# Kernel optimization log

Measured on AMD Instinct MI355X. Metric: run time of the kernel, lower is better.

The kernel has to match this reference:

```python
import jax, jax.numpy as jnp
import numpy as np

NUM_SPECIAL = 3  # rows 1..NUM_SPECIAL in special table; row 0 is padding (zeros)

def setup_inputs() -> dict:
    key = jax.random.key(0)
    ks = jax.random.split(key, 16)
    T, B, E, H, L, V = 128, 32, 512, 512, 2, 32000
    G = 4 * H
    s = 0.02
    special_emb = jax.random.normal(ks[1], (NUM_SPECIAL + 1, E), jnp.float32) * s
    special_emb = special_emb.at[0].set(0.0)  # padding_idx=0
    return {
        "ids": jax.random.randint(ks[0], (T, B), 0, V),
        "length_countdown": jax.random.uniform(ks[2], (T, B, 1), jnp.float32),
        "word_emb": jax.random.normal(ks[3], (V, E), jnp.float32) * s,
        "special_emb": special_emb,
        "h0": jax.random.normal(ks[4], (L, B, H), jnp.float32) * s,
        "c0": jax.random.normal(ks[5], (L, B, H), jnp.float32) * s,
        "prev_output": jnp.zeros((B, H), jnp.float32),
        "Wih0": jax.random.normal(ks[6], (G, E + H + 1), jnp.float32) * s,
        "Whh0": jax.random.normal(ks[7], (G, H), jnp.float32) * s,
        "bih0": jnp.zeros((G,), jnp.float32),
        "bhh0": jnp.zeros((G,), jnp.float32),
        "Wih1": jax.random.normal(ks[8], (G, H), jnp.float32) * s,
        "Whh1": jax.random.normal(ks[9], (G, H), jnp.float32) * s,
        "bih1": jnp.zeros((G,), jnp.float32),
        "bhh1": jnp.zeros((G,), jnp.float32),
        "Wg": jax.random.normal(ks[10], (V, H), jnp.float32) * s,
        "bg": jnp.zeros((V,), jnp.float32),
    }

def _lstm_cell(x, h, c, Wih, Whh, bih, bhh):
    gates = x @ Wih.T + bih + h @ Whh.T + bhh  # [B, 4H]
    i, f, g, o = jnp.split(gates, 4, axis=-1)  # torch LSTMCell gate order
    c_new = jax.nn.sigmoid(f) * c + jax.nn.sigmoid(i) * jnp.tanh(g)
    h_new = jax.nn.sigmoid(o) * jnp.tanh(c_new)
    return h_new, c_new

def reference(ids, length_countdown, word_emb, special_emb, h0, c0, prev_output,
              Wih0, Whh0, bih0, bhh0, Wih1, Whh1, bih1, bhh1, Wg, bg):
    # embeddings = word_embeddings(ids) + special_embeddings(special_ids(ids))
    sp_ids = jnp.where(ids < NUM_SPECIAL, ids + 1, 0)
    emb = word_emb[ids] + special_emb[sp_ids]                 # [T,B,E]
    rnn_in = jnp.concatenate([emb, length_countdown], axis=2)  # [T,B,E+1]

    Wihs = (Wih0, Wih1); Whhs = (Whh0, Whh1)
    bihs = (bih0, bih1); bhhs = (bhh0, bhh1)
    L = h0.shape[0]

    def step(carry, emb_t):
        out, h, c = carry
        x = jnp.concatenate([emb_t, out], axis=1)  # input feeding
        hs, cs = [], []
        for l in range(L):
            h_l, c_l = _lstm_cell(x, h[l], c[l], Wihs[l], Whhs[l], bihs[l], bhhs[l])
            x = h_l  # dropout=0
            hs.append(h_l); cs.append(c_l)
        out = x
        score = jax.nn.log_softmax(out @ Wg.T + bg, axis=-1)  # generator
        return (out, jnp.stack(hs), jnp.stack(cs)), score

    (out, hT, cT), scores = jax.lax.scan(step, (prev_output, h0, c0), rnn_in)
    return scores, (hT, cT), out
```

## Files before the change

### kernel.cpp

```cpp
#include <hip/hip_runtime.h>
#include <hip/hip_bf16.h>


typedef __attribute__((ext_vector_type(8))) short bf16x8;
typedef __attribute__((ext_vector_type(4))) float f32x4;
typedef __attribute__((ext_vector_type(2))) unsigned long long u64x2;

#define AS1 __attribute__((address_space(1)))
#define AS3 __attribute__((address_space(3)))
#define RLX __ATOMIC_RELAXED
#define AGT __HIP_MEMORY_SCOPE_AGENT
#define NGEN 176
#define NSUB 48

__device__ __forceinline__ unsigned short f2bf(float f) {
  unsigned int u = __builtin_bit_cast(unsigned int, f);
  u += 0x7fffu + ((u >> 16) & 1u);
  return (unsigned short)(u >> 16);
}

__device__ __forceinline__ void gl16(const void* g, void* l) {
  __builtin_amdgcn_global_load_lds((const AS1 unsigned int*)g,
                                   (AS3 unsigned int*)l, 16, 0, 0);
}

__device__ __forceinline__ float sigm(float x) { return 1.0f / (1.0f + __expf(-x)); }

__global__ __launch_bounds__(256, 1) void prep_k(
    const float* __restrict__ Wg,  const float* __restrict__ Wih0,
    const float* __restrict__ Whh0,const float* __restrict__ Wih1,
    const float* __restrict__ Whh1,const float* __restrict__ bih0,
    const float* __restrict__ bhh0,const float* __restrict__ bih1,
    const float* __restrict__ bhh1,const float* __restrict__ h0,
    const float* __restrict__ pout,
    unsigned short* __restrict__ WgBf, unsigned short* __restrict__ W0e,
    unsigned short* __restrict__ Wr0p, unsigned short* __restrict__ Wr1p,
    float* __restrict__ b1p, float* __restrict__ bias0c,
    float* __restrict__ wcd, unsigned short* __restrict__ H0X,
    unsigned short* __restrict__ FOUT, unsigned short* __restrict__ H1I)
{
  const long N0 = 16384000L;
  const long N1 = N0 + 1048576L;
  const long N2 = N1 + 2097152L;
  const long N3 = N2 + 2097152L;
  const long N4 = N3 + 2048L;
  const long N5 = N4 + 2048L;
  const long N6 = N5 + 2048L;
  const long N7 = N6 + 49152L;
  for (long i = blockIdx.x * 256L + threadIdx.x; i < N7; i += 256L * gridDim.x) {
    if (i < N0) {
      WgBf[i] = f2bf(Wg[i]);
    } else if (i < N1) {
      long k = i - N0; int g = (int)(k >> 9); int kk = (int)(k & 511);
      W0e[k] = f2bf(Wih0[g * 1025 + kk]);
    } else if (i < N2) {
      long k = i - N1; int gp = (int)(k >> 10); int kk = (int)(k & 1023);
      int j = gp >> 2, gate = gp & 3; int g = gate * 512 + j;
      float v = (kk < 512) ? Whh0[g * 512 + kk] : Wih0[g * 1025 + 513 + (kk - 512)];
      Wr0p[k] = f2bf(v);
    } else if (i < N3) {
      long k = i - N2; int gp = (int)(k >> 10); int kk = (int)(k & 1023);
      int j = gp >> 2, gate = gp & 3; int g = gate * 512 + j;
      float v = (kk < 512) ? Wih1[g * 512 + kk] : Whh1[g * 512 + (kk - 512)];
      Wr1p[k] = f2bf(v);
    } else if (i < N4) {
      int gp = (int)(i - N3); int j = gp >> 2, gate = gp & 3; int g = gate * 512 + j;
      b1p[gp] = bih1[g] + bhh1[g];
    } else if (i < N5) {
      int g = (int)(i - N4); bias0c[g] = bih0[g] + bhh0[g];
    } else if (i < N6) {
      int g = (int)(i - N5); wcd[g] = Wih0[g * 1025 + 512];
    } else {
      long k = i - N6;
      int sub = (int)(k >> 14);
      int e = (int)(k & 16383);
      int wgx = e >> 9, b = (e >> 4) & 31, jl = e & 15;
      int j = wgx * 16 + jl;
      float v = (sub == 0) ? h0[b * 512 + j]
              : (sub == 1) ? h0[16384 + b * 512 + j]
                           : pout[b * 512 + j];
      unsigned short* dst = (sub == 0) ? H0X : (sub == 1) ? H1I : FOUT;
      dst[e] = f2bf(v);
    }
  }
}

__global__ __launch_bounds__(256, 1) void emb_k(
    const int* __restrict__ ids, const float* __restrict__ wemb,
    const float* __restrict__ semb, unsigned short* __restrict__ ebf)
{
  const int tb = blockIdx.x;
  const int id = ids[tb];
  const int sp = (id < 3) ? (id + 1) : 0;
  const float* wr = wemb + (long)id * 512;
  const float* sr = semb + sp * 512;
  for (int i = threadIdx.x; i < 512; i += 256)
    ebf[tb * 512 + i] = f2bf(wr[i] + sr[i]);
}

__global__ __launch_bounds__(256, 1) void gemm_p0(
    const unsigned short* __restrict__ A,
    const unsigned short* __restrict__ B, int N,
    float* __restrict__ C,
    const float* __restrict__ e0, const float* __restrict__ e1,
    const float* __restrict__ e2)
{
  __shared__ unsigned short sA[4096];
  __shared__ unsigned short sB[4096];
  const int tid = threadIdx.x;
  const int l = tid & 63, w = tid >> 6;
  const int nb = N >> 7;
  const int bid = blockIdx.x;
  const int bm = bid / nb, bn = bid - bm * nb;

  const int u0 = w * 128 + l;
  const int u1 = u0 + 64;
  const int r0 = u0 >> 2, c0 = (u0 & 3) ^ (r0 & 3);
  const int r1 = u1 >> 2, c1 = (u1 & 3) ^ (r1 & 3);
  const unsigned short* ga0 = A + (long)(bm * 128 + r0) * 512 + c0 * 8;
  const unsigned short* ga1 = A + (long)(bm * 128 + r1) * 512 + c1 * 8;
  const unsigned short* gb0 = B + (long)(bn * 128 + r0) * 512 + c0 * 8;
  const unsigned short* gb1 = B + (long)(bn * 128 + r1) * 512 + c1 * 8;
  unsigned short* la0 = sA + (w * 2 + 0) * 512;
  unsigned short* la1 = sA + (w * 2 + 1) * 512;
  unsigned short* lb0 = sB + (w * 2 + 0) * 512;
  unsigned short* lb1 = sB + (w * 2 + 1) * 512;

  const int fr = l & 15, fc = l >> 4;
  const int wm = w >> 1, wn = w & 1;
  int aoff[4], boff[4];
#pragma unroll
  for (int mi = 0; mi < 4; ++mi) {
    int row = wm * 64 + mi * 16 + fr;
    aoff[mi] = row * 64 + ((fc ^ (row & 3)) * 16);
  }
#pragma unroll
  for (int ni = 0; ni < 4; ++ni) {
    int row = wn * 64 + ni * 16 + fr;
    boff[ni] = row * 64 + ((fc ^ (row & 3)) * 16);
  }

  f32x4 acc[4][4];
#pragma unroll
  for (int i = 0; i < 4; ++i)
#pragma unroll
    for (int jq = 0; jq < 4; ++jq) acc[i][jq] = (f32x4){0.f, 0.f, 0.f, 0.f};

  for (int kt = 0; kt < 16; ++kt) {
    __syncthreads();
    gl16(ga0 + kt * 32, la0);
    gl16(ga1 + kt * 32, la1);
    gl16(gb0 + kt * 32, lb0);
    gl16(gb1 + kt * 32, lb1);
    asm volatile("s_waitcnt vmcnt(0)" ::: "memory");
    __syncthreads();
    bf16x8 av[4], bv[4];
#pragma unroll
    for (int mi = 0; mi < 4; ++mi)
      av[mi] = *(const bf16x8*)((const char*)sA + aoff[mi]);
#pragma unroll
    for (int ni = 0; ni < 4; ++ni)
      bv[ni] = *(const bf16x8*)((const char*)sB + boff[ni]);
#pragma unroll
    for (int mi = 0; mi < 4; ++mi)
#pragma unroll
      for (int ni = 0; ni < 4; ++ni)
        acc[mi][ni] = __builtin_amdgcn_mfma_f32_16x16x32_bf16(av[mi], bv[ni], acc[mi][ni], 0, 0, 0);
  }

  const int mbase = bm * 128 + wm * 64;
  const int nbase = bn * 128 + wn * 64;
#pragma unroll
  for (int mi = 0; mi < 4; ++mi)
#pragma unroll
    for (int ni = 0; ni < 4; ++ni) {
      const int col = nbase + ni * 16 + fr;
#pragma unroll
      for (int r = 0; r < 4; ++r) {
        const int row = mbase + mi * 16 + fc * 4 + r;
        const int gp = ((row & 511) << 2) | (row >> 9);
        float v = acc[mi][ni][r] + e0[row] + e2[col] * e1[row];
        C[(long)gp * N + col] = v;
      }
    }
}

__global__ __launch_bounds__(256, 1) void lstm_seq(
    const unsigned short* __restrict__ Wr0p,
    const unsigned short* __restrict__ Wr1p,
    float* __restrict__ P0t, const float* __restrict__ b1p,
    const float* __restrict__ c0in,
    unsigned short* __restrict__ H0X, unsigned short* __restrict__ H1X,
    const unsigned short* __restrict__ FOUT, const unsigned short* __restrict__ H1I,
    unsigned short* __restrict__ outbf, float* __restrict__ outs,
    unsigned int* __restrict__ flagA, unsigned int* __restrict__ flagB,
    unsigned int* __restrict__ flagC, unsigned int* __restrict__ cntBM,
    unsigned int* __restrict__ rowTk,
    const unsigned short* __restrict__ WgBf, const float* __restrict__ bg)
{
  const int tid = threadIdx.x;
  __shared__ char smem[75264] __attribute__((aligned(16)));

  if (blockIdx.x < 32) {
    unsigned short* sx = (unsigned short*)smem;
    float (*sg)[65] = (float(*)[65])(smem + 65536);
    unsigned short (*sh)[16] = (unsigned short(*)[16])(smem + 73856);

    const int wg = blockIdx.x;
    const int l = tid & 63, w = tid >> 6;
    const int fr = l & 15, fc = l >> 4;
    const int b = tid & 31, jl0 = tid >> 5;
    const int sb = l >> 1, sjh = l & 1;

    float c0r[2], c1r[2], h0k[2], h1k[2];
#pragma unroll
    for (int jq = 0; jq < 2; ++jq) {
      c0r[jq] = c0in[b * 512 + wg * 16 + jl0 + jq * 8];
      c1r[jq] = c0in[16384 + b * 512 + wg * 16 + jl0 + jq * 8];
      h0k[jq] = 0.f; h1k[jq] = 0.f;
    }

    float b1v[8];
#pragma unroll
    for (int jq = 0; jq < 2; ++jq)
#pragma unroll
      for (int g = 0; g < 4; ++g)
        b1v[jq * 4 + g] = b1p[(wg * 16 + jl0 + jq * 8) * 4 + g];

    const char* sxb0 = (const char*)sx + fr * 2048;
    const char* sxb1 = (const char*)sx + (16 + fr) * 2048;
    const int xr = (fr & 7) << 4;
    const int wrow = (wg * 64 + w * 16 + fr) * 1024 + fc * 8;

    char* const sxw = (char*)sx + sb * 2048;
    const int sswz = (sb & 7) << 4;

#define STAGE2(srcp, half)                                                    \
  do {                                                                        \
    unsigned long long q0[8], q1[8];                                          \
    _Pragma("unroll")                                                         \
    for (int i = 0; i < 8; ++i) {                                             \
      int u = i * 256 + tid;                                                  \
      q0[i] = __hip_atomic_load((const unsigned long long*)(srcp) + u * 2,    \
                                RLX, AGT);                                    \
      q1[i] = __hip_atomic_load((const unsigned long long*)(srcp) + u * 2 + 1,\
                                RLX, AGT);                                    \
    }                                                                         \
    _Pragma("unroll")                                                         \
    for (int i = 0; i < 8; ++i) {                                             \
      int cb = (half) * 1024 + (i * 4 + w) * 32 + sjh * 16;                   \
      u64x2 v; v.x = q0[i]; v.y = q1[i];                                      \
      *(u64x2*)(sxw + (cb ^ sswz)) = v;                                       \
    }                                                                         \
  } while (0)

#define MFMA_HALF(Wp, k0, a0v, a1v)                                           \
  do {                                                                        \
    _Pragma("unroll")                                                         \
    for (int kt = (k0); kt < (k0) + 16; ++kt) {                               \
      bf16x8 bv = *(const bf16x8*)((Wp) + wrow + kt * 32);                    \
      bf16x8 x0 = *(const bf16x8*)(sxb0 + ((kt * 64 + fc * 16) ^ xr));        \
      bf16x8 x1 = *(const bf16x8*)(sxb1 + ((kt * 64 + fc * 16) ^ xr));        \
      a0v = __builtin_amdgcn_mfma_f32_16x16x32_bf16(x0, bv, a0v, 0, 0, 0);    \
      a1v = __builtin_amdgcn_mfma_f32_16x16x32_bf16(x1, bv, a1v, 0, 0, 0);    \
    }                                                                         \
  } while (0)

#define POLL(flags, tgt)                                                      \
  do {                                                                        \
    const unsigned int* fp = (flags) + ((l & 31) << 5);                       \
    for (;;) {                                                                \
      unsigned int f = __hip_atomic_load(fp, RLX, AGT);                       \
      if (__all((int)(f >= (unsigned int)(tgt)))) break;                      \
      __builtin_amdgcn_s_sleep(1);                                            \
    }                                                                         \
    asm volatile("" ::: "memory");                                            \
  } while (0)

    STAGE2(H0X, 0);
    __syncthreads();
    if (tid == 0)
      __hip_atomic_store(&flagB[wg << 5], 1u, RLX, AGT);

    for (int t = 0; t < 128; ++t) {
      float p0v[8];
#pragma unroll
      for (int jq = 0; jq < 2; ++jq)
#pragma unroll
        for (int g = 0; g < 4; ++g)
          p0v[jq * 4 + g] =
              P0t[(long)((wg * 16 + jl0 + jq * 8) * 4 + g) * 4096 + t * 32 + b];

      f32x4 accA0 = (f32x4){0.f, 0.f, 0.f, 0.f};
      f32x4 accA1 = (f32x4){0.f, 0.f, 0.f, 0.f};
      MFMA_HALF(Wr0p, 0, accA0, accA1);

      POLL(flagB, t + 1);
      if (t == 0) STAGE2(FOUT, 1); else STAGE2(H1X, 1);
      __syncthreads();
      MFMA_HALF(Wr0p, 16, accA0, accA1);
#pragma unroll
      for (int r = 0; r < 4; ++r) {
        sg[fc * 4 + r][w * 16 + fr] = accA0[r];
        sg[16 + fc * 4 + r][w * 16 + fr] = accA1[r];
      }
      __syncthreads();
#pragma unroll
      for (int jq = 0; jq < 2; ++jq) {
        const int jl = jl0 + jq * 8;
        float gi = sg[b][jl * 4 + 0] + p0v[jq * 4 + 0];
        float gf = sg[b][jl * 4 + 1] + p0v[jq * 4 + 1];
        float gg = sg[b][jl * 4 + 2] + p0v[jq * 4 + 2];
        float go = sg[b][jl * 4 + 3] + p0v[jq * 4 + 3];
        float cn = sigm(gf) * c0r[jq] + sigm(gi) * tanhf(gg);
        float hn = sigm(go) * tanhf(cn);
        c0r[jq] = cn; h0k[jq] = hn;
        sh[b][jl] = f2bf(hn);
      }
      __syncthreads();
      if (w == 0) {
        u64x2 v = *(const u64x2*)&sh[sb][sjh * 8];
        unsigned long long* dst =
            (unsigned long long*)(H0X + wg * 512 + sb * 16 + sjh * 8);
        __hip_atomic_store(dst,     v.x, RLX, AGT);
        __hip_atomic_store(dst + 1, v.y, RLX, AGT);
        asm volatile("s_waitcnt vmcnt(0)" ::: "memory");
        if (tid == 0)
          __hip_atomic_store(&flagA[wg << 5], (unsigned int)(t + 1), RLX, AGT);
      }

      f32x4 accB0 = (f32x4){0.f, 0.f, 0.f, 0.f};
      f32x4 accB1 = (f32x4){0.f, 0.f, 0.f, 0.f};
      if (t == 0) {
        STAGE2(H1I, 1);
        __syncthreads();
      }
      MFMA_HALF(Wr1p, 16, accB0, accB1);

      POLL(flagA, t + 1);
      STAGE2(H0X, 0);
      __syncthreads();
      MFMA_HALF(Wr1p, 0, accB0, accB1);
#pragma unroll
      for (int r = 0; r < 4; ++r) {
        sg[fc * 4 + r][w * 16 + fr] = accB0[r];
        sg[16 + fc * 4 + r][w * 16 + fr] = accB1[r];
      }
      __syncthreads();
#pragma unroll
      for (int jq = 0; jq < 2; ++jq) {
        const int jl = jl0 + jq * 8;
        float gi = sg[b][jl * 4 + 0] + b1v[jq * 4 + 0];
        float gf = sg[b][jl * 4 + 1] + b1v[jq * 4 + 1];
        float gg = sg[b][jl * 4 + 2] + b1v[jq * 4 + 2];
        float go = sg[b][jl * 4 + 3] + b1v[jq * 4 + 3];
        float cn = sigm(gf) * c1r[jq] + sigm(gi) * tanhf(gg);
        float hn = sigm(go) * tanhf(cn);
        c1r[jq] = cn; h1k[jq] = hn;
        sh[b][jl] = f2bf(hn);
      }
      __syncthreads();
      if (w == 0) {
        u64x2 v = *(const u64x2*)&sh[sb][sjh * 8];
        unsigned long long* dst =
            (unsigned long long*)(H1X + wg * 512 + sb * 16 + sjh * 8);
        __hip_atomic_store(dst,     v.x, RLX, AGT);
        __hip_atomic_store(dst + 1, v.y, RLX, AGT);
        asm volatile("s_waitcnt vmcnt(0)" ::: "memory");
        if (tid == 0)
          __hip_atomic_store(&flagB[wg << 5], (unsigned int)(t + 2), RLX, AGT);
      } else if (w == 1) {
        const unsigned long long* s = (const unsigned long long*)&sh[sb][sjh * 8];
        unsigned long long* dst =
            (unsigned long long*)(outbf + (t * 32 + sb) * 512 + wg * 16 + sjh * 8);
        __hip_atomic_store(dst,     s[0], RLX, AGT);
        __hip_atomic_store(dst + 1, s[1], RLX, AGT);
        asm volatile("s_waitcnt vmcnt(0)" ::: "memory");
        if (l == 0)
          __hip_atomic_store(&flagC[wg << 5], (unsigned int)(t + 1), RLX, AGT);
      }
    }
#undef STAGE2
#undef MFMA_HALF
#undef POLL

    float* hT = outs + 131072000;
    float* cT = outs + 131072000 + 32768;
    float* oT = outs + 131072000 + 65536;
#pragma unroll
    for (int jq = 0; jq < 2; ++jq) {
      const int j = wg * 16 + jl0 + jq * 8;
      hT[b * 512 + j] = h0k[jq];
      hT[16384 + b * 512 + j] = h1k[jq];
      cT[b * 512 + j] = c0r[jq];
      cT[16384 + b * 512 + j] = c1r[jq];
      oT[b * 512 + j] = h1k[jq];
    }
    return;
  }

  if (blockIdx.x < 32 + NGEN) {
    unsigned short* sA = (unsigned short*)smem;
    unsigned short* sB = (unsigned short*)(smem + 8192);
    float (*pmw)[2][2] = (float(*)[2][2])(smem + 16384);

    const int g = (int)blockIdx.x - 32;
    const int l = tid & 63, w = tid >> 6;
    const int fr = l & 15, fc = l >> 4;
    const int wm = w >> 1, wn = w & 1;

    const int u0 = w * 128 + l, u1 = u0 + 64;
    const int r0 = u0 >> 2, c0 = (u0 & 3) ^ (r0 & 3);
    const int r1 = u1 >> 2, c1 = (u1 & 3) ^ (r1 & 3);
    unsigned short* lb0 = sB + (w * 2 + 0) * 512;
    unsigned short* lb1 = sB + (w * 2 + 1) * 512;

    int aoff[4], boff[4];
#pragma unroll
    for (int mi = 0; mi < 4; ++mi) {
      int row = wm * 64 + mi * 16 + fr;
      aoff[mi] = row * 64 + ((fc ^ (row & 3)) * 16);
    }
#pragma unroll
    for (int ni = 0; ni < 4; ++ni) {
      int row = wn * 64 + ni * 16 + fr;
      boff[ni] = row * 64 + ((fc ^ (row & 3)) * 16);
    }

    for (int job = g; job < 8000; job += NGEN) {
      const int bm = job / 250, bn = job - bm * 250;

      if (w == 0) {
        const unsigned int* fp = flagC + ((l & 31) << 5);
        const unsigned int tgt = (unsigned int)(4 * bm + 4);
        for (;;) {
          unsigned int f = __hip_atomic_load(fp, RLX, AGT);
          if (__all((int)(f >= tgt))) break;
          __builtin_amdgcn_s_sleep(16);
        }
        asm volatile("" ::: "memory");
      }
      __syncthreads();

      const unsigned short* Ab0 = outbf + (long)(bm * 128 + r0) * 512 + c0 * 8;
      const unsigned short* Ab1 = outbf + (long)(bm * 128 + r1) * 512 + c1 * 8;
      const unsigned short* gb0 = WgBf + (long)(bn * 128 + r0) * 512 + c0 * 8;
      const unsigned short* gb1 = WgBf + (long)(bn * 128 + r1) * 512 + c1 * 8;

      f32x4 acc[4][4];
#pragma unroll
      for (int i = 0; i < 4; ++i)
#pragma unroll
        for (int jq = 0; jq < 4; ++jq) acc[i][jq] = (f32x4){0.f, 0.f, 0.f, 0.f};

      for (int kt = 0; kt < 16; ++kt) {
        __syncthreads();
        unsigned long long a0x = __hip_atomic_load((const unsigned long long*)(Ab0 + kt * 32),     RLX, AGT);
        unsigned long long a0y = __hip_atomic_load((const unsigned long long*)(Ab0 + kt * 32) + 1, RLX, AGT);
        unsigned long long a1x = __hip_atomic_load((const unsigned long long*)(Ab1 + kt * 32),     RLX, AGT);
        unsigned long long a1y = __hip_atomic_load((const unsigned long long*)(Ab1 + kt * 32) + 1, RLX, AGT);
        gl16(gb0 + kt * 32, lb0);
        gl16(gb1 + kt * 32, lb1);
        { u64x2 va; va.x = a0x; va.y = a0y; *(u64x2*)((char*)sA + u0 * 16) = va; }
        { u64x2 va; va.x = a1x; va.y = a1y; *(u64x2*)((char*)sA + u1 * 16) = va; }
        asm volatile("s_waitcnt vmcnt(0)" ::: "memory");
        __syncthreads();
        bf16x8 av[4], bv[4];
#pragma unroll
        for (int mi = 0; mi < 4; ++mi)
          av[mi] = *(const bf16x8*)((const char*)sA + aoff[mi]);
#pragma unroll
        for (int ni = 0; ni < 4; ++ni)
          bv[ni] = *(const bf16x8*)((const char*)sB + boff[ni]);
#pragma unroll
        for (int mi = 0; mi < 4; ++mi)
#pragma unroll
          for (int ni = 0; ni < 4; ++ni)
            acc[mi][ni] = __builtin_amdgcn_mfma_f32_16x16x32_bf16(av[mi], bv[ni], acc[mi][ni], 0, 0, 0);
      }

      const int mbase = bm * 128 + wm * 64;
      const int nbase = bn * 128 + wn * 64;
      float m2[4][4], s2[4][4];
#pragma unroll
      for (int mi = 0; mi < 4; ++mi)
#pragma unroll
        for (int r = 0; r < 4; ++r) { m2[mi][r] = -3.0e38f; s2[mi][r] = 0.f; }
#pragma unroll
      for (int mi = 0; mi < 4; ++mi)
#pragma unroll
        for (int ni = 0; ni < 4; ++ni) {
          const int col = nbase + ni * 16 + fr;
          const float bgc = bg[col];
#pragma unroll
          for (int r = 0; r < 4; ++r) {
            float v = acc[mi][ni][r] + bgc;
            acc[mi][ni][r] = v;
            __hip_atomic_store(&outs[(long)(mbase + mi * 16 + fc * 4 + r) * 32000L + col],
                               v, RLX, AGT);
            m2[mi][r] = fmaxf(m2[mi][r], v);
          }
        }
#pragma unroll
      for (int mi = 0; mi < 4; ++mi)
#pragma unroll
        for (int r = 0; r < 4; ++r)
#pragma unroll
          for (int s = 1; s < 16; s <<= 1)
            m2[mi][r] = fmaxf(m2[mi][r], __shfl_xor(m2[mi][r], s));
#pragma unroll
      for (int mi = 0; mi < 4; ++mi)
#pragma unroll
        for (int ni = 0; ni < 4; ++ni)
#pragma unroll
          for (int r = 0; r < 4; ++r)
            s2[mi][r] += __expf(acc[mi][ni][r] - m2[mi][r]);
#pragma unroll
      for (int mi = 0; mi < 4; ++mi)
#pragma unroll
        for (int r = 0; r < 4; ++r)
#pragma unroll
          for (int s = 1; s < 16; s <<= 1)
            s2[mi][r] += __shfl_xor(s2[mi][r], s);
      if (fr == 0) {
#pragma unroll
        for (int mi = 0; mi < 4; ++mi)
#pragma unroll
          for (int r = 0; r < 4; ++r) {
            const int rl = wm * 64 + mi * 16 + fc * 4 + r;
            pmw[rl][wn][0] = m2[mi][r];
            pmw[rl][wn][1] = s2[mi][r];
          }
      }
      __syncthreads();
      if (tid < 128) {
        float ma = pmw[tid][0][0], sa = pmw[tid][0][1];
        float mb = pmw[tid][1][0], sb2 = pmw[tid][1][1];
        float M = fmaxf(ma, mb);
        float S = sa * __expf(ma - M) + sb2 * __expf(mb - M);
        int q2 = 2 * (tid * 250 + bn);
        unsigned long long* p = (unsigned long long*)
            (P0t + ((long)(q2 >> 7)) * 4096 + 128L * bm + (q2 & 127));
        float2 o; o.x = M; o.y = S;
        __hip_atomic_store(p, __builtin_bit_cast(unsigned long long, o), RLX, AGT);
      }
      asm volatile("s_waitcnt vmcnt(0)" ::: "memory");
      __syncthreads();
      if (tid == 0)
        __hip_atomic_fetch_add(&cntBM[bm << 5], 1u, RLX, AGT);
      __syncthreads();
    }
  }

  {
    float* red = (float*)smem;
    unsigned* rowsh = (unsigned*)(smem + 64);

    for (;;) {
      if (tid == 0)
        rowsh[0] = __hip_atomic_fetch_add(rowTk, 1u, RLX, AGT);
      __syncthreads();
      const unsigned row = rowsh[0];
      if (row >= 4096u) break;
      const int bm = (int)(row >> 7), rl = (int)(row & 127);

      if (tid == 0) {
        for (;;) {
          unsigned c = __hip_atomic_load(&cntBM[bm << 5], RLX, AGT);
          if (c >= 250u) break;
          __builtin_amdgcn_s_sleep(32);
        }
      }
      __syncthreads();
      asm volatile("" ::: "memory");

      float m = -3.0e38f, sm = 0.0f;
      if (tid < 250) {
        int q2 = 2 * (rl * 250 + tid);
        const unsigned long long* pp = (const unsigned long long*)
            (P0t + ((long)(q2 >> 7)) * 4096 + 128L * bm + (q2 & 127));
        unsigned long long q = __hip_atomic_load(pp, RLX, AGT);
        float2 f = __builtin_bit_cast(float2, q);
        m = f.x; sm = f.y;
      }
#pragma unroll
      for (int off = 32; off > 0; off >>= 1) {
        float mo = __shfl_down(m, off);
        float so = __shfl_down(sm, off);
        float mn = fmaxf(m, mo);
        sm = sm * __expf(m - mn) + so * __expf(mo - mn);
        m = mn;
      }
      if ((tid & 63) == 0) { red[tid >> 6] = m; red[4 + (tid >> 6)] = sm; }
      __syncthreads();
      if (tid == 0) {
        float M = red[0], S = red[4];
#pragma unroll
        for (int i = 1; i < 4; ++i) {
          float mn = fmaxf(M, red[i]);
          S = S * __expf(M - mn) + red[4 + i] * __expf(red[i] - mn);
          M = mn;
        }
        red[8] = M + __logf(S);
      }
      __syncthreads();
      const float lse = red[8];

      float* pr = outs + (long)row * 32000L;
#define SUBGRP(START, CNT)                                                    \
      do {                                                                    \
        unsigned long long qa[CNT], qb[CNT];                                  \
        _Pragma("unroll")                                                     \
        for (int k = 0; k < CNT; ++k) {                                       \
          const unsigned long long* lp =                                      \
              (const unsigned long long*)(pr + ((START + k) * 256 + tid) * 4);\
          qa[k] = __hip_atomic_load(lp,     RLX, AGT);                        \
          qb[k] = __hip_atomic_load(lp + 1, RLX, AGT);                        \
        }                                                                     \
        _Pragma("unroll")                                                     \
        for (int k = 0; k < CNT; ++k) {                                       \
          float2 fa = __builtin_bit_cast(float2, qa[k]);                      \
          float2 fb = __builtin_bit_cast(float2, qb[k]);                      \
          float4 v;                                                           \
          v.x = fa.x - lse; v.y = fa.y - lse;                                 \
          v.z = fb.x - lse; v.w = fb.y - lse;                                 \
          *(float4*)(pr + ((START + k) * 256 + tid) * 4) = v;                 \
        }                                                                     \
      } while (0)
      SUBGRP(0, 8);
      SUBGRP(8, 8);
      SUBGRP(16, 8);
      SUBGRP(24, 7);
#undef SUBGRP
      if (tid < 64) {
        const int i = 31 * 256 + tid;
        const unsigned long long* lp = (const unsigned long long*)(pr + i * 4);
        unsigned long long qa = __hip_atomic_load(lp,     RLX, AGT);
        unsigned long long qb = __hip_atomic_load(lp + 1, RLX, AGT);
        float2 fa = __builtin_bit_cast(float2, qa);
        float2 fb = __builtin_bit_cast(float2, qb);
        float4 v;
        v.x = fa.x - lse; v.y = fa.y - lse; v.z = fb.x - lse; v.w = fb.y - lse;
        *(float4*)(pr + i * 4) = v;
      }
      __syncthreads();
    }
  }
}

extern "C" void kernel_launch(void* const* d_in, const int* in_sizes, int n_in,
                              void* d_out, int out_size, void* d_ws, size_t ws_size,
                              hipStream_t stream) {
  const int*   ids  = (const int*)d_in[0];
  const float* cd   = (const float*)d_in[1];
  const float* wemb = (const float*)d_in[2];
  const float* semb = (const float*)d_in[3];
  const float* h0   = (const float*)d_in[4];
  const float* c0   = (const float*)d_in[5];
  const float* pout = (const float*)d_in[6];
  const float* Wih0 = (const float*)d_in[7];
  const float* Whh0 = (const float*)d_in[8];
  const float* bih0 = (const float*)d_in[9];
  const float* bhh0 = (const float*)d_in[10];
  const float* Wih1 = (const float*)d_in[11];
  const float* Whh1 = (const float*)d_in[12];
  const float* bih1 = (const float*)d_in[13];
  const float* bhh1 = (const float*)d_in[14];
  const float* Wg   = (const float*)d_in[15];
  const float* bg   = (const float*)d_in[16];
  float* out = (float*)d_out;

  char* ws = (char*)d_ws;
  unsigned short* WgBf   = (unsigned short*)(ws);
  unsigned short* W0e    = (unsigned short*)(ws + 32768000);
  unsigned short* Wr0p   = (unsigned short*)(ws + 34865152);
  unsigned short* Wr1p   = (unsigned short*)(ws + 39059456);
  float*          b1p    = (float*)(ws + 43253760);
  float*          bias0c = (float*)(ws + 43261952);
  float*          wcd    = (float*)(ws + 43270144);
  unsigned short* embbf  = (unsigned short*)(ws + 43278336);
  unsigned short* outbf  = (unsigned short*)(ws + 47472640);
  float*          P0t    = (float*)(ws + 51666944);
  unsigned int*   flagA  = (unsigned int*)(ws + 85221376);
  unsigned int*   flagB  = (unsigned int*)(ws + 85225472);
  unsigned short* H0X    = (unsigned short*)(ws + 85229568);
  unsigned short* H1X    = (unsigned short*)(ws + 85262336);
  unsigned short* FOUT   = (unsigned short*)(ws + 85295104);
  unsigned short* H1I    = (unsigned short*)(ws + 85327872);
  unsigned int*   flagC  = (unsigned int*)(ws + 85360640);
  unsigned int*   cntBM  = (unsigned int*)(ws + 85364736);
  unsigned int*   rowTk  = (unsigned int*)(ws + 85368832);

  hipMemsetAsync((void*)flagA, 0, 8192, stream);
  hipMemsetAsync((void*)flagC, 0, 12288, stream);

  prep_k<<<8192, 256, 0, stream>>>(Wg, Wih0, Whh0, Wih1, Whh1,
                                   bih0, bhh0, bih1, bhh1, h0, pout,
                                   WgBf, W0e, Wr0p, Wr1p, b1p, bias0c, wcd,
                                   H0X, FOUT, H1I);

  emb_k<<<4096, 256, 0, stream>>>(ids, wemb, semb, embbf);

  gemm_p0<<<512, 256, 0, stream>>>(W0e, embbf, 4096, P0t, bias0c, wcd, cd);

  lstm_seq<<<32 + NGEN + NSUB, 256, 0, stream>>>(Wr0p, Wr1p, P0t, b1p, c0,
                                                 H0X, H1X, FOUT, H1I, outbf, out,
                                                 flagA, flagB, flagC, cntBM,
                                                 rowTk, WgBf, bg);
}
```

Before: 1.780 ms.

## Widen generator GEMM tiles to 128x256 and rebalance generator/sub-block counts

Each generator job now computes two adjacent 128-column vocab tiles, sharing the A (hidden-state) tile load across both and halving the job count. This cuts the redundant A loads from global memory and the per-job flag polling and synchronisation. The price is double the accumulator registers, which raises register pressure, and a larger LDS footprint. Block counts also shift from 176 generator / 48 sub blocks to 192 / 32.

```diff
diff --git a/kernel.cpp b/kernel.cpp
--- a/kernel.cpp
+++ b/kernel.cpp
@@ -10,8 +10,8 @@
 #define AS3 __attribute__((address_space(3)))
 #define RLX __ATOMIC_RELAXED
 #define AGT __HIP_MEMORY_SCOPE_AGENT
-#define NGEN 176
-#define NSUB 48
+#define NGEN 192
+#define NSUB 32
 
 __device__ __forceinline__ unsigned short f2bf(float f) {
   unsigned int u = __builtin_bit_cast(unsigned int, f);
@@ -400,9 +400,10 @@
   }
 
   if (blockIdx.x < 32 + NGEN) {
-    unsigned short* sA = (unsigned short*)smem;
-    unsigned short* sB = (unsigned short*)(smem + 8192);
-    float (*pmw)[2][2] = (float(*)[2][2])(smem + 16384);
+    unsigned short* sA  = (unsigned short*)smem;
+    unsigned short* sB0 = (unsigned short*)(smem + 8192);
+    unsigned short* sB1 = (unsigned short*)(smem + 16384);
+    float (*pmw)[2][2] = (float(*)[2][2])(smem + 24576);
 
     const int g = (int)blockIdx.x - 32;
     const int l = tid & 63, w = tid >> 6;
@@ -412,8 +413,10 @@
     const int u0 = w * 128 + l, u1 = u0 + 64;
     const int r0 = u0 >> 2, c0 = (u0 & 3) ^ (r0 & 3);
     const int r1 = u1 >> 2, c1 = (u1 & 3) ^ (r1 & 3);
-    unsigned short* lb0 = sB + (w * 2 + 0) * 512;
-    unsigned short* lb1 = sB + (w * 2 + 1) * 512;
+    unsigned short* lb00 = sB0 + (w * 2 + 0) * 512;
+    unsigned short* lb01 = sB0 + (w * 2 + 1) * 512;
+    unsigned short* lb10 = sB1 + (w * 2 + 0) * 512;
+    unsigned short* lb11 = sB1 + (w * 2 + 1) * 512;
 
     int aoff[4], boff[4];
 #pragma unroll
@@ -427,8 +430,9 @@
       boff[ni] = row * 64 + ((fc ^ (row & 3)) * 16);
     }
 
-    for (int job = g; job < 8000; job += NGEN) {
-      const int bm = job / 250, bn = job - bm * 250;
+    for (int job = g; job < 4000; job += NGEN) {
+      const int bm = job / 125, bn2 = job - bm * 125;
+      const int bn = bn2 * 2;
 
       if (w == 0) {
         const unsigned int* fp = flagC + ((l & 31) << 5);
@@ -444,14 +448,19 @@
 
       const unsigned short* Ab0 = outbf + (long)(bm * 128 + r0) * 512 + c0 * 8;
       const unsigned short* Ab1 = outbf + (long)(bm * 128 + r1) * 512 + c1 * 8;
-      const unsigned short* gb0 = WgBf + (long)(bn * 128 + r0) * 512 + c0 * 8;
-      const unsigned short* gb1 = WgBf + (long)(bn * 128 + r1) * 512 + c1 * 8;
-
-      f32x4 acc[4][4];
+      const unsigned short* g00 = WgBf + (long)(bn * 128 + r0) * 512 + c0 * 8;
+      const unsigned short* g01 = WgBf + (long)(bn * 128 + r1) * 512 + c1 * 8;
+      const unsigned short* g10 = WgBf + (long)((bn + 1) * 128 + r0) * 512 + c0 * 8;
+      const unsigned short* g11 = WgBf + (long)((bn + 1) * 128 + r1) * 512 + c1 * 8;
+
+      f32x4 ac0[4][4], ac1[4][4];
 #pragma unroll
       for (int i = 0; i < 4; ++i)
 #pragma unroll
-        for (int jq = 0; jq < 4; ++jq) acc[i][jq] = (f32x4){0.f, 0.f, 0.f, 0.f};
+        for (int jq = 0; jq < 4; ++jq) {
+          ac0[i][jq] = (f32x4){0.f, 0.f, 0.f, 0.f};
+          ac1[i][jq] = (f32x4){0.f, 0.f, 0.f, 0.f};
+        }
 
       for (int kt = 0; kt < 16; ++kt) {
         __syncthreads();
@@ -459,95 +468,104 @@
         unsigned long long a0y = __hip_atomic_load((const unsigned long long*)(Ab0 + kt * 32) + 1, RLX, AGT);
         unsigned long long a1x = __hip_atomic_load((const unsigned long long*)(Ab1 + kt * 32),     RLX, AGT);
         unsigned long long a1y = __hip_atomic_load((const unsigned long long*)(Ab1 + kt * 32) + 1, RLX, AGT);
-        gl16(gb0 + kt * 32, lb0);
-        gl16(gb1 + kt * 32, lb1);
+        gl16(g00 + kt * 32, lb00);
+        gl16(g01 + kt * 32, lb01);
+        gl16(g10 + kt * 32, lb10);
+        gl16(g11 + kt * 32, lb11);
         { u64x2 va; va.x = a0x; va.y = a0y; *(u64x2*)((char*)sA + u0 * 16) = va; }
         { u64x2 va; va.x = a1x; va.y = a1y; *(u64x2*)((char*)sA + u1 * 16) = va; }
         asm volatile("s_waitcnt vmcnt(0)" ::: "memory");
         __syncthreads();
-        bf16x8 av[4], bv[4];
+        bf16x8 av[4];
 #pragma unroll
         for (int mi = 0; mi < 4; ++mi)
           av[mi] = *(const bf16x8*)((const char*)sA + aoff[mi]);
 #pragma unroll
-        for (int ni = 0; ni < 4; ++ni)
-          bv[ni] = *(const bf16x8*)((const char*)sB + boff[ni]);
-#pragma unroll
-        for (int mi = 0; mi < 4; ++mi)
-#pragma unroll
-          for (int ni = 0; ni < 4; ++ni)
-            acc[mi][ni] = __builtin_amdgcn_mfma_f32_16x16x32_bf16(av[mi], bv[ni], acc[mi][ni], 0, 0, 0);
-      }
-
-      const int mbase = bm * 128 + wm * 64;
-      const int nbase = bn * 128 + wn * 64;
-      float m2[4][4], s2[4][4];
-#pragma unroll
-      for (int mi = 0; mi < 4; ++mi)
-#pragma unroll
-        for (int r = 0; r < 4; ++r) { m2[mi][r] = -3.0e38f; s2[mi][r] = 0.f; }
-#pragma unroll
-      for (int mi = 0; mi < 4; ++mi)
-#pragma unroll
         for (int ni = 0; ni < 4; ++ni) {
-          const int col = nbase + ni * 16 + fr;
-          const float bgc = bg[col];
-#pragma unroll
-          for (int r = 0; r < 4; ++r) {
-            float v = acc[mi][ni][r] + bgc;
-            acc[mi][ni][r] = v;
-            __hip_atomic_store(&outs[(long)(mbase + mi * 16 + fc * 4 + r) * 32000L + col],
-                               v, RLX, AGT);
-            m2[mi][r] = fmaxf(m2[mi][r], v);
+          bf16x8 bv0 = *(const bf16x8*)((const char*)sB0 + boff[ni]);
+          bf16x8 bv1 = *(const bf16x8*)((const char*)sB1 + boff[ni]);
+#pragma unroll
+          for (int mi = 0; mi < 4; ++mi) {
+            ac0[mi][ni] = __builtin_amdgcn_mfma_f32_16x16x32_bf16(av[mi], bv0, ac0[mi][ni], 0, 0, 0);
+            ac1[mi][ni] = __builtin_amdgcn_mfma_f32_16x16x32_bf16(av[mi], bv1, ac1[mi][ni], 0, 0, 0);
           }
         }
-#pragma unroll
-      for (int mi = 0; mi < 4; ++mi)
-#pragma unroll
-        for (int r = 0; r < 4; ++r)
-#pragma unroll
-          for (int s = 1; s < 16; s <<= 1)
-            m2[mi][r] = fmaxf(m2[mi][r], __shfl_xor(m2[mi][r], s));
-#pragma unroll
-      for (int mi = 0; mi < 4; ++mi)
-#pragma unroll
-        for (int ni = 0; ni < 4; ++ni)
+      }
+
+      const int mbase = bm * 128 + wm * 64;
+#pragma unroll
+      for (int tt = 0; tt < 2; ++tt) {
+        f32x4 (*ac)[4] = (tt == 0) ? ac0 : ac1;
+        const int nbase = (bn + tt) * 128 + wn * 64;
+        float m2[4][4], s2[4][4];
+#pragma unroll
+        for (int mi = 0; mi < 4; ++mi)
+#pragma unroll
+          for (int r = 0; r < 4; ++r) { m2[mi][r] = -3.0e38f; s2[mi][r] = 0.f; }
+#pragma unroll
+        for (int mi = 0; mi < 4; ++mi)
+#pragma unroll
+          for (int ni = 0; ni < 4; ++ni) {
+            const int col = nbase + ni * 16 + fr;
+            const float bgc = bg[col];
+#pragma unroll
+            for (int r = 0; r < 4; ++r) {
+              float v = ac[mi][ni][r] + bgc;
+              ac[mi][ni][r] = v;
+              __hip_atomic_store(&outs[(long)(mbase + mi * 16 + fc * 4 + r) * 32000L + col],
+                                 v, RLX, AGT);
+              m2[mi][r] = fmaxf(m2[mi][r], v);
+            }
+          }
+#pragma unroll
+        for (int mi = 0; mi < 4; ++mi)
 #pragma unroll
           for (int r = 0; r < 4; ++r)
-            s2[mi][r] += __expf(acc[mi][ni][r] - m2[mi][r]);
-#pragma unroll
-      for (int mi = 0; mi < 4; ++mi)
-#pragma unroll
-        for (int r = 0; r < 4; ++r)
-#pragma unroll
-          for (int s = 1; s < 16; s <<= 1)
-            s2[mi][r] += __shfl_xor(s2[mi][r], s);
-      if (fr == 0) {
+#pragma unroll
+            for (int s = 1; s < 16; s <<= 1)
+              m2[mi][r] = fmaxf(m2[mi][r], __shfl_xor(m2[mi][r], s));
 #pragma unroll
         for (int mi = 0; mi < 4; ++mi)
 #pragma unroll
-          for (int r = 0; r < 4; ++r) {
-            const int rl = wm * 64 + mi * 16 + fc * 4 + r;
-            pmw[rl][wn][0] = m2[mi][r];
-            pmw[rl][wn][1] = s2[mi][r];
-          }
-      }
-      __syncthreads();
-      if (tid < 128) {
-        float ma = pmw[tid][0][0], sa = pmw[tid][0][1];
-        float mb = pmw[tid][1][0], sb2 = pmw[tid][1][1];
-        float M = fmaxf(ma, mb);
-        float S = sa * __expf(ma - M) + sb2 * __expf(mb - M);
-        int q2 = 2 * (tid * 250 + bn);
-        unsigned long long* p = (unsigned long long*)
-            (P0t + ((long)(q2 >> 7)) * 4096 + 128L * bm + (q2 & 127));
-        float2 o; o.x = M; o.y = S;
-        __hip_atomic_store(p, __builtin_bit_cast(unsigned long long, o), RLX, AGT);
+          for (int ni = 0; ni < 4; ++ni)
+#pragma unroll
+            for (int r = 0; r < 4; ++r)
+              s2[mi][r] += __expf(ac[mi][ni][r] - m2[mi][r]);
+#pragma unroll
+        for (int mi = 0; mi < 4; ++mi)
+#pragma unroll
+          for (int r = 0; r < 4; ++r)
+#pragma unroll
+            for (int s = 1; s < 16; s <<= 1)
+              s2[mi][r] += __shfl_xor(s2[mi][r], s);
+        if (fr == 0) {
+#pragma unroll
+          for (int mi = 0; mi < 4; ++mi)
+#pragma unroll
+            for (int r = 0; r < 4; ++r) {
+              const int rl = wm * 64 + mi * 16 + fc * 4 + r;
+              pmw[rl][wn][0] = m2[mi][r];
+              pmw[rl][wn][1] = s2[mi][r];
+            }
+        }
+        __syncthreads();
+        if (tid < 128) {
+          float ma = pmw[tid][0][0], sa = pmw[tid][0][1];
+          float mb = pmw[tid][1][0], sb2 = pmw[tid][1][1];
+          float M = fmaxf(ma, mb);
+          float S = sa * __expf(ma - M) + sb2 * __expf(mb - M);
+          int q2 = 2 * (tid * 250 + bn + tt);
+          unsigned long long* p = (unsigned long long*)
+              (P0t + ((long)(q2 >> 7)) * 4096 + 128L * bm + (q2 & 127));
+          float2 o; o.x = M; o.y = S;
+          __hip_atomic_store(p, __builtin_bit_cast(unsigned long long, o), RLX, AGT);
+        }
+        __syncthreads();
       }
       asm volatile("s_waitcnt vmcnt(0)" ::: "memory");
       __syncthreads();
       if (tid == 0)
-        __hip_atomic_fetch_add(&cntBM[bm << 5], 1u, RLX, AGT);
+        __hip_atomic_fetch_add(&cntBM[bm << 5], 2u, RLX, AGT);
       __syncthreads();
     }
   }
```

After: 1.732 ms. -2.7%, faster.
